# Optimization experiments

Measured on AMD Instinct MI355X. Metric: run time of the kernel, lower is better.

Reference implementation:

```python
import jax, jax.numpy as jnp
import numpy as np

B, Q, C, P, A = 32, 300, 81, 300, 29


def box_cxcywh_to_xyxy(b):
    cx, cy, w, h = b[..., 0], b[..., 1], b[..., 2], b[..., 3]
    return jnp.stack([cx - 0.5 * w, cy - 0.5 * h, cx + 0.5 * w, cy + 0.5 * h], axis=-1)


def setup_inputs() -> dict:
    key = jax.random.key(0)
    k1, k2, k3, k4, k5 = jax.random.split(key, 5)
    pred_logits = jax.random.normal(k1, (B, Q, C), dtype=jnp.float32)
    pred_boxes = jax.random.uniform(k2, (B, Q, 4), dtype=jnp.float32)
    pred_actions = jax.random.normal(k3, (B, P, A), dtype=jnp.float32)
    pred_rel_pairs = jax.random.randint(k4, (B, P, 2), 0, Q, dtype=jnp.int64)
    # realistic image sizes (h, w) in pixels
    target_sizes = 480.0 + 320.0 * jax.random.uniform(k5, (B, 2), dtype=jnp.float32)
    return {
        'pred_logits': pred_logits,
        'pred_boxes': pred_boxes,
        'pred_actions': pred_actions,
        'pred_rel_pairs': pred_rel_pairs,
        'target_sizes': target_sizes,
    }


def reference(pred_logits, pred_boxes, pred_actions, pred_rel_pairs, target_sizes):
    threshold = 0.0
    # class scores/labels (last class is no-object, excluded from max)
    prob = jax.nn.softmax(pred_logits, axis=-1)
    scores = prob[..., :-1].max(-1)          # [B,Q]
    labels = prob[..., :-1].argmax(-1)       # [B,Q]
    # boxes to xyxy, scaled to image size
    boxes = box_cxcywh_to_xyxy(pred_boxes)   # [B,Q,4]
    img_h, img_w = target_sizes[:, 0], target_sizes[:, 1]
    scale_fct = jnp.stack([img_w, img_h, img_w, img_h], axis=1)  # [B,4]
    boxes = boxes * scale_fct[:, None, :]
    # vcoco path: pairwise action score matrix via one fused scatter
    pair_actions = jax.nn.sigmoid(pred_actions)          # [B,P,A]
    h_idx = pred_rel_pairs[:, :, 0]                      # [B,P]
    o_idx = pred_rel_pairs[:, :, 1]                      # [B,P]
    # original: if h_idx == o_idx -> o_idx = -1 (i.e. last column K of K+1)
    o_idx = jnp.where(h_idx == o_idx, Q, o_idx)
    b_idx = jnp.arange(B, dtype=h_idx.dtype)[:, None]    # [B,1] -> broadcast [B,P]
    score = jnp.zeros((B, Q, Q + 1, A), dtype=pair_actions.dtype)
    score = score.at[b_idx, h_idx, o_idx].set(pair_actions)
    score = jnp.transpose(score, (0, 3, 1, 2))           # [B,A,Q,Q+1]
    # ragged boolean masks (returned as masks instead of data-dependent slices)
    h_mask = (labels == 1) & (scores > threshold)        # human rows
    o_mask = jnp.concatenate([scores > threshold,
                              jnp.ones((B, 1), dtype=bool)], axis=1)  # K+1 cols
    return scores, labels, boxes, score, h_mask, o_mask
```

## Files before the change

### kernel.cpp

```cpp
#include <hip/hip_runtime.h>
#include <hip/hip_bf16.h>

#define BB 32
#define QQ 300
#define CC 81
#define PP 300
#define AA 29

constexpr long long OFF_SCORES = 0;
constexpr long long OFF_LABELS = OFF_SCORES + (long long)BB * QQ;
constexpr long long OFF_BOXES  = OFF_LABELS + (long long)BB * QQ;
constexpr long long OFF_SCORE  = OFF_BOXES  + (long long)BB * QQ * 4;
constexpr long long SCORE_ELEMS = (long long)BB * AA * QQ * (QQ + 1);
constexpr long long OFF_HMASK  = OFF_SCORE + SCORE_ELEMS;
constexpr long long OFF_OMASK  = OFF_HMASK + (long long)BB * QQ;

__global__ void cls_box_mask_kernel(const float* __restrict__ logits,
                                    const float* __restrict__ boxes_in,
                                    const float* __restrict__ tsize,
                                    float* __restrict__ out) {
    int t = blockIdx.x * blockDim.x + threadIdx.x;
    if (t >= BB * QQ) return;
    int b = t / QQ;
    int q = t - b * QQ;

    const float* l = logits + (long long)t * CC;

    float m = -1e30f;
    float best = -1e30f;
    int am = 0;
    for (int c = 0; c < CC; ++c) {
        float x = l[c];
        m = fmaxf(m, x);
        if (c < CC - 1 && x > best) { best = x; am = c; }
    }
    float s = 0.0f;
    for (int c = 0; c < CC; ++c) {
        s += __expf(l[c] - m);
    }
    float score = __expf(best - m) / s;

    out[OFF_SCORES + t] = score;
    out[OFF_LABELS + t] = (float)am;

    float cx = boxes_in[4 * (long long)t + 0];
    float cy = boxes_in[4 * (long long)t + 1];
    float w  = boxes_in[4 * (long long)t + 2];
    float h  = boxes_in[4 * (long long)t + 3];
    float img_h = tsize[2 * b + 0];
    float img_w = tsize[2 * b + 1];
    out[OFF_BOXES + 4 * (long long)t + 0] = (cx - 0.5f * w) * img_w;
    out[OFF_BOXES + 4 * (long long)t + 1] = (cy - 0.5f * h) * img_h;
    out[OFF_BOXES + 4 * (long long)t + 2] = (cx + 0.5f * w) * img_w;
    out[OFF_BOXES + 4 * (long long)t + 3] = (cy + 0.5f * h) * img_h;

    out[OFF_HMASK + t] = (am == 1 && score > 0.0f) ? 1.0f : 0.0f;
    out[OFF_OMASK + (long long)b * (QQ + 1) + q] = (score > 0.0f) ? 1.0f : 0.0f;
    if (q == 0) out[OFF_OMASK + (long long)b * (QQ + 1) + QQ] = 1.0f;
}

__global__ void scatter_kernel(const int* __restrict__ pairs,
                               const float* __restrict__ actions,
                               float* __restrict__ out) {
    __shared__ int keys[PP];
    __shared__ int nz;
    int tid = threadIdx.x;
    if (tid == 0) nz = 0;
    __syncthreads();

    int local = 0;
    for (int i = tid; i < BB * PP; i += blockDim.x) local |= pairs[2 * i + 1];
    if (local) atomicOr(&nz, 1);
    __syncthreads();
    bool is64 = (nz == 0);

    int b = blockIdx.x;
    int p = tid;
    int h = -1, o = -1;
    if (p < PP) {
        if (is64) {
            h = pairs[((long long)(b * PP + p)) * 4 + 0];
            o = pairs[((long long)(b * PP + p)) * 4 + 2];
        } else {
            h = pairs[((long long)(b * PP + p)) * 2 + 0];
            o = pairs[((long long)(b * PP + p)) * 2 + 1];
        }
        if (h == o) o = QQ;
        keys[p] = h * (QQ + 1) + o;
    }
    __syncthreads();
    if (p >= PP) return;

    int k = keys[p];
    for (int p2 = p + 1; p2 < PP; ++p2) {
        if (keys[p2] == k) return;
    }

    const float* act = actions + (long long)(b * PP + p) * AA;
    long long base = OFF_SCORE + (long long)b * AA * QQ * (QQ + 1)
                   + (long long)h * (QQ + 1) + o;
    for (int a = 0; a < AA; ++a) {
        float x = act[a];
        float sg = 1.0f / (1.0f + __expf(-x));
        out[base + (long long)a * QQ * (QQ + 1)] = sg;
    }
}

extern "C" void kernel_launch(void* const* d_in, const int* in_sizes, int n_in,
                              void* d_out, int out_size, void* d_ws, size_t ws_size,
                              hipStream_t stream) {
    const float* logits   = (const float*)d_in[0];
    const float* boxes_in = (const float*)d_in[1];
    const float* actions  = (const float*)d_in[2];
    const int*   pairs    = (const int*)d_in[3];
    const float* tsize    = (const float*)d_in[4];
    float* out = (float*)d_out;

    hipMemsetAsync((char*)d_out + OFF_SCORE * sizeof(float), 0,
                   (size_t)SCORE_ELEMS * sizeof(float), stream);

    int n = BB * QQ;
    cls_box_mask_kernel<<<(n + 255) / 256, 256, 0, stream>>>(logits, boxes_in, tsize, out);
    scatter_kernel<<<BB, 320, 0, stream>>>(pairs, actions, out);
}
```

Measured before the change: 396.4 us.

## Fuse zero-fill of score tensor into classification kernel with nontemporal vector stores

Replaces the separate memset of the large pairwise score tensor with a grid-stride zero-fill inside the classification/box kernel, using 16-byte nontemporal stores. It also vectorizes the box load and store. This removes one operation launch and aims to keep the fill bandwidth-efficient without polluting caches. The risk is that a hand-written fill with a fixed grid of 2048 blocks may reach lower write bandwidth than the driver memset.

```diff
diff --git a/kernel.cpp b/kernel.cpp
--- a/kernel.cpp
+++ b/kernel.cpp
@@ -15,19 +15,31 @@
 constexpr long long OFF_HMASK  = OFF_SCORE + SCORE_ELEMS;
 constexpr long long OFF_OMASK  = OFF_HMASK + (long long)BB * QQ;
 
-__global__ void cls_box_mask_kernel(const float* __restrict__ logits,
-                                    const float* __restrict__ boxes_in,
-                                    const float* __restrict__ tsize,
-                                    float* __restrict__ out) {
-    int t = blockIdx.x * blockDim.x + threadIdx.x;
-    if (t >= BB * QQ) return;
+typedef float floatx4 __attribute__((ext_vector_type(4)));
+
+__global__ __launch_bounds__(256) void fill_cls_kernel(
+        const float* __restrict__ logits,
+        const float* __restrict__ boxes_in,
+        const float* __restrict__ tsize,
+        float* __restrict__ out) {
+    long long tid = (long long)blockIdx.x * blockDim.x + threadIdx.x;
+    long long nthreads = (long long)gridDim.x * blockDim.x;
+
+    floatx4* dst = (floatx4*)(out + OFF_SCORE);
+    const long long n4 = SCORE_ELEMS / 4;
+    floatx4 z = {0.0f, 0.0f, 0.0f, 0.0f};
+    for (long long i = tid; i < n4; i += nthreads) {
+        __builtin_nontemporal_store(z, &dst[i]);
+    }
+
+    if (tid >= BB * QQ) return;
+    int t = (int)tid;
     int b = t / QQ;
     int q = t - b * QQ;
 
     const float* l = logits + (long long)t * CC;
 
-    float m = -1e30f;
-    float best = -1e30f;
+    float m = -1e30f, best = -1e30f;
     int am = 0;
     for (int c = 0; c < CC; ++c) {
         float x = l[c];
@@ -35,24 +47,21 @@
         if (c < CC - 1 && x > best) { best = x; am = c; }
     }
     float s = 0.0f;
-    for (int c = 0; c < CC; ++c) {
-        s += __expf(l[c] - m);
-    }
+    for (int c = 0; c < CC; ++c) s += __expf(l[c] - m);
     float score = __expf(best - m) / s;
 
     out[OFF_SCORES + t] = score;
     out[OFF_LABELS + t] = (float)am;
 
-    float cx = boxes_in[4 * (long long)t + 0];
-    float cy = boxes_in[4 * (long long)t + 1];
-    float w  = boxes_in[4 * (long long)t + 2];
-    float h  = boxes_in[4 * (long long)t + 3];
+    floatx4 bx = *(const floatx4*)(boxes_in + 4 * (long long)t);
     float img_h = tsize[2 * b + 0];
     float img_w = tsize[2 * b + 1];
-    out[OFF_BOXES + 4 * (long long)t + 0] = (cx - 0.5f * w) * img_w;
-    out[OFF_BOXES + 4 * (long long)t + 1] = (cy - 0.5f * h) * img_h;
-    out[OFF_BOXES + 4 * (long long)t + 2] = (cx + 0.5f * w) * img_w;
-    out[OFF_BOXES + 4 * (long long)t + 3] = (cy + 0.5f * h) * img_h;
+    floatx4 r;
+    r.x = (bx.x - 0.5f * bx.z) * img_w;
+    r.y = (bx.y - 0.5f * bx.w) * img_h;
+    r.z = (bx.x + 0.5f * bx.z) * img_w;
+    r.w = (bx.y + 0.5f * bx.w) * img_h;
+    *(floatx4*)(out + OFF_BOXES + 4 * (long long)t) = r;
 
     out[OFF_HMASK + t] = (am == 1 && score > 0.0f) ? 1.0f : 0.0f;
     out[OFF_OMASK + (long long)b * (QQ + 1) + q] = (score > 0.0f) ? 1.0f : 0.0f;
@@ -116,10 +125,6 @@
     const float* tsize    = (const float*)d_in[4];
     float* out = (float*)d_out;
 
-    hipMemsetAsync((char*)d_out + OFF_SCORE * sizeof(float), 0,
-                   (size_t)SCORE_ELEMS * sizeof(float), stream);
-
-    int n = BB * QQ;
-    cls_box_mask_kernel<<<(n + 255) / 256, 256, 0, stream>>>(logits, boxes_in, tsize, out);
+    fill_cls_kernel<<<2048, 256, 0, stream>>>(logits, boxes_in, tsize, out);
     scatter_kernel<<<BB, 320, 0, stream>>>(pairs, actions, out);
 }
```

New measurement: 423.5 us. +6.8%, slower.
